# Optimization experiments

Hardware: AMD Instinct MI355X
Metric: run time of the kernel (lower is better)

## Reference

```python
import jax, jax.numpy as jnp
import numpy as np

N = 4096      # n_nodes
IN = 256      # in_features
H = 4         # n_heads
F = 64        # out_features (per head)
SLOPE = 0.2   # leaky relu negative slope


def setup_inputs() -> dict:
    key = jax.random.key(0)
    k0, k1, k2, k3 = jax.random.split(key, 4)
    h = jax.random.normal(k0, (N, IN), dtype=jnp.float32)
    adj = jax.random.randint(k1, (N, N), 0, 2, dtype=jnp.int32)
    # ensure every node has at least one neighbor (self-loop) so softmax is defined
    adj = jnp.maximum(adj, jnp.eye(N, dtype=jnp.int32))
    # linear: in_features -> out_features * n_heads (xavier-ish scale)
    W = jax.random.normal(k2, (H * F, IN), dtype=jnp.float32) * np.float32(1.0 / np.sqrt(IN))
    b = jnp.zeros((H * F,), dtype=jnp.float32)
    # attn: Linear(2*F -> 1), weight row vector of size 2F plus scalar bias
    attn_w = jax.random.normal(k3, (2 * F,), dtype=jnp.float32) * np.float32(1.0 / np.sqrt(2 * F))
    attn_b = jnp.zeros((1,), dtype=jnp.float32)
    return {"h": h, "adj_mat": adj, "W": W, "b": b, "attn_w": attn_w, "attn_b": attn_b}


def reference(h, adj_mat, W, b, attn_w, attn_b):
    n = h.shape[0]
    # node projection: [N, H, F]
    g = (h @ W.T + b).reshape(n, H, F)
    # attn(concat(h_i, h_j)) = <a_src, g_i> + <a_dst, g_j> + bias  (decomposed, same math)
    src = jnp.einsum('nhf,f->nh', g, attn_w[:F])   # [N, H] contribution of node i
    dst = jnp.einsum('nhf,f->nh', g, attn_w[F:])   # [N, H] contribution of node j
    e = src[:, None, :] + dst[None, :, :] + attn_b[0]   # [N, N, H]
    e = jnp.where(e >= 0, e, SLOPE * e)                 # leaky relu
    e = jnp.where(adj_mat[:, :, None] != 0, e, -jnp.inf)  # mask non-edges
    a = jax.nn.softmax(e, axis=1)                       # softmax over neighbors j
    out = jnp.einsum('ijh,jhf->ihf', a, g)              # [N, H, F]
    return out.mean(axis=1)                             # average heads -> [N, F]
```

## Files before the change

### kernel.cpp

```cpp
#include <hip/hip_runtime.h>
#include <stdint.h>

constexpr int NODES = 4096;
constexpr int KIN   = 256;
constexpr int NHEAD = 4;
constexpr int NF    = 64;
constexpr int HFQ   = 256;
#define SLOPE 0.2f
#define L2E 1.44269504088896340736f

typedef __attribute__((ext_vector_type(8))) short short8;
typedef __attribute__((ext_vector_type(4))) float floatx4;

static __device__ __forceinline__ unsigned short f2bf(float f) {
  return __builtin_bit_cast(unsigned short, (__bf16)f);
}

__global__ __launch_bounds__(256) void prep_kernel(
    const float* __restrict__ hin, const float* __restrict__ Win,
    unsigned short* __restrict__ hB, unsigned short* __restrict__ WB) {
  int idx = blockIdx.x * 256 + threadIdx.x;
  const int NH4 = (NODES * KIN) / 4;
  const int NW4 = (HFQ * KIN) / 4;
  if (idx < NH4) {
    float4 v = reinterpret_cast<const float4*>(hin)[idx];
    ushort4 o = { f2bf(v.x), f2bf(v.y), f2bf(v.z), f2bf(v.w) };
    reinterpret_cast<ushort4*>(hB)[idx] = o;
  } else if (idx < NH4 + NW4) {
    int j = idx - NH4;
    float4 v = reinterpret_cast<const float4*>(Win)[j];
    ushort4 o = { f2bf(v.x), f2bf(v.y), f2bf(v.z), f2bf(v.w) };
    reinterpret_cast<ushort4*>(WB)[j] = o;
  }
}

__global__ __launch_bounds__(256) void proj_kernel(
    const unsigned short* __restrict__ hB, const unsigned short* __restrict__ WB,
    const float* __restrict__ bias,
    float* __restrict__ g32, unsigned short* __restrict__ gT) {
  int wave = threadIdx.x >> 6, lane = threadIdx.x & 63;
  int tile = blockIdx.x * 4 + wave;
  int mt = tile >> 4, nt = tile & 15;
  int m0 = mt * 16, n0 = nt * 16;
  int r = lane & 15, kg = lane >> 4;
  floatx4 acc = {0.f, 0.f, 0.f, 0.f};
  const short8* Ap = reinterpret_cast<const short8*>(hB + (m0 + r) * KIN + kg * 8);
  const short8* Bp = reinterpret_cast<const short8*>(WB + (n0 + r) * KIN + kg * 8);
#pragma unroll
  for (int kb = 0; kb < 8; ++kb) {
    short8 a = Ap[kb * 4];
    short8 b = Bp[kb * 4];
    acc = __builtin_amdgcn_mfma_f32_16x16x32_bf16(a, b, acc, 0, 0, 0);
  }
  int col = n0 + r;
  float bv = bias[col];
#pragma unroll
  for (int q = 0; q < 4; ++q) {
    int row = m0 + kg * 4 + q;
    float v = acc[q] + bv;
    g32[row * HFQ + col] = v;
    gT[col * NODES + row] = f2bf(v);
  }
}

__global__ __launch_bounds__(256) void srcdst_kernel(
    const float* __restrict__ g32, const float* __restrict__ attn_w,
    const float* __restrict__ attn_b,
    float* __restrict__ src, float* __restrict__ dst) {
  int wave = threadIdx.x >> 6, lane = threadIdx.x & 63;
  int n = blockIdx.x * 4 + wave;
  float aws = attn_w[lane], awd = attn_w[64 + lane];
  float ab = attn_b[0];
#pragma unroll
  for (int hh = 0; hh < NHEAD; ++hh) {
    float v = g32[n * HFQ + hh * NF + lane];
    float s = v * aws, d = v * awd;
#pragma unroll
    for (int m = 32; m >= 1; m >>= 1) {
      s += __shfl_xor(s, m, 64);
      d += __shfl_xor(d, m, 64);
    }
    if (lane == 0) {
      src[n * NHEAD + hh] = s + ab;
      dst[n * NHEAD + hh] = d;
    }
  }
}

__global__ __launch_bounds__(256) void attn_kernel(
    const int* __restrict__ adj, const unsigned short* __restrict__ gT,
    const float* __restrict__ src, const float* __restrict__ dst,
    float* __restrict__ pnum, float* __restrict__ pden, int JP) {
  extern __shared__ char smem[];
  unsigned short* gTl = reinterpret_cast<unsigned short*>(smem);
  float* dstL = reinterpret_cast<float*>(smem + 256 * 80);
  int tid = threadIdx.x;
  int wave = tid >> 6, lane = tid & 63;
  int row_in = lane & 15, kg = lane >> 4;
  int part = blockIdx.y;
  int jstart = part * JP;
  int arow = blockIdx.x * 64 + wave * 16 + row_in;

  for (int idx = tid; idx < NHEAD * JP; idx += 256) {
    int hh = idx / JP, jl = idx - hh * JP;
    dstL[hh * JP + jl] = dst[(jstart + jl) * NHEAD + hh];
  }

  float srcv[NHEAD];
#pragma unroll
  for (int hh = 0; hh < NHEAD; ++hh) srcv[hh] = src[arow * NHEAD + hh];

  floatx4 acc[NHEAD][4];
#pragma unroll
  for (int hh = 0; hh < NHEAD; ++hh)
#pragma unroll
    for (int ft = 0; ft < 4; ++ft) acc[hh][ft] = floatx4{0.f, 0.f, 0.f, 0.f};
  float den[NHEAD] = {0.f, 0.f, 0.f, 0.f};

  __syncthreads();

  int nsteps = JP / 32;
  for (int stp = 0; stp < nsteps; ++stp) {
    int j0l = stp * 32;
    int jg = jstart + j0l;
#pragma unroll
    for (int it = 0; it < 4; ++it) {
      int q = it * 256 + tid;
      int c = q >> 2, jc = q & 3;
      short8 v = *reinterpret_cast<const short8*>(gT + c * NODES + jg + jc * 8);
      *reinterpret_cast<short8*>(gTl + c * 40 + jc * 8) = v;
    }
    int base_adj = arow * NODES + jg + kg * 8;
    int4 a01 = *reinterpret_cast<const int4*>(adj + base_adj);
    int4 a23 = *reinterpret_cast<const int4*>(adj + base_adj + 4);
    __syncthreads();
#pragma unroll
    for (int hh = 0; hh < NHEAD; ++hh) {
      const float* dl = dstL + hh * JP + j0l + kg * 8;
      float4 d01 = *reinterpret_cast<const float4*>(dl);
      float4 d23 = *reinterpret_cast<const float4*>(dl + 4);
      float dv[8] = {d01.x, d01.y, d01.z, d01.w, d23.x, d23.y, d23.z, d23.w};
      int av[8] = {a01.x, a01.y, a01.z, a01.w, a23.x, a23.y, a23.z, a23.w};
      float dsum = 0.f;
      short8 afr;
#pragma unroll
      for (int rr = 0; rr < 8; ++rr) {
        float t = srcv[hh] + dv[rr];
        float u = fmaxf(t, SLOPE * t);
        float p = exp2f(u * L2E);
        float wv = (av[rr] != 0) ? p : 0.f;
        dsum += wv;
        afr[rr] = (short)f2bf(wv);
      }
      den[hh] += dsum;
#pragma unroll
      for (int ft = 0; ft < 4; ++ft) {
        int c = hh * NF + ft * 16 + row_in;
        short8 bfr = *reinterpret_cast<const short8*>(gTl + c * 40 + kg * 8);
        acc[hh][ft] = __builtin_amdgcn_mfma_f32_16x16x32_bf16(afr, bfr, acc[hh][ft], 0, 0, 0);
      }
    }
    __syncthreads();
  }

#pragma unroll
  for (int hh = 0; hh < NHEAD; ++hh) {
    den[hh] += __shfl_xor(den[hh], 16, 64);
    den[hh] += __shfl_xor(den[hh], 32, 64);
  }
  if (kg == 0) {
#pragma unroll
    for (int hh = 0; hh < NHEAD; ++hh)
      pden[part * (NODES * NHEAD) + arow * NHEAD + hh] = den[hh];
  }
#pragma unroll
  for (int hh = 0; hh < NHEAD; ++hh)
#pragma unroll
    for (int ft = 0; ft < 4; ++ft)
#pragma unroll
      for (int q = 0; q < 4; ++q) {
        int row = blockIdx.x * 64 + wave * 16 + kg * 4 + q;
        int col = hh * NF + ft * 16 + row_in;
        pnum[part * (NODES * HFQ) + row * HFQ + col] = acc[hh][ft][q];
      }
}

__global__ __launch_bounds__(256) void combine_kernel(
    const float* __restrict__ pnum, const float* __restrict__ pden,
    float* __restrict__ out, int NP) {
  int idx = blockIdx.x * 256 + threadIdx.x;
  int i = idx >> 6, f = idx & 63;
  float o = 0.f;
#pragma unroll
  for (int hh = 0; hh < NHEAD; ++hh) {
    float num = 0.f, den = 0.f;
    for (int p = 0; p < NP; ++p) {
      num += pnum[p * (NODES * HFQ) + i * HFQ + hh * NF + f];
      den += pden[p * (NODES * NHEAD) + i * NHEAD + hh];
    }
    o += num / den;
  }
  out[idx] = 0.25f * o;
}

extern "C" void kernel_launch(void* const* d_in, const int* in_sizes, int n_in,
                              void* d_out, int out_size, void* d_ws, size_t ws_size,
                              hipStream_t stream) {
  const float* hin = (const float*)d_in[0];
  const int* adj   = (const int*)d_in[1];
  const float* W   = (const float*)d_in[2];
  const float* b   = (const float*)d_in[3];
  const float* aw  = (const float*)d_in[4];
  const float* ab  = (const float*)d_in[5];
  float* out = (float*)d_out;
  char* ws = (char*)d_ws;

  unsigned short* hB  = (unsigned short*)(ws + 0x000000);
  unsigned short* WB  = (unsigned short*)(ws + 0x200000);
  float* g32          = (float*)(ws + 0x400000);
  unsigned short* gT  = (unsigned short*)(ws + 0x800000);
  float* src          = (float*)(ws + 0xA00000);
  float* dst          = (float*)(ws + 0xA10000);
  float* pden         = (float*)(ws + 0xA30000);
  float* pnum         = (float*)(ws + 0xB00000);
  const size_t base = 0xB00000;

  int NP = 2;
  if (ws_size >= base + 8ull * NODES * HFQ * 4) NP = 8;
  else if (ws_size >= base + 4ull * NODES * HFQ * 4) NP = 4;
  int JP = NODES / NP;

  prep_kernel<<<1088, 256, 0, stream>>>(hin, W, hB, WB);
  proj_kernel<<<1024, 256, 0, stream>>>(hB, WB, b, g32, gT);
  srcdst_kernel<<<1024, 256, 0, stream>>>(g32, aw, ab, src, dst);
  size_t smem = 256 * 80 + (size_t)NHEAD * JP * 4;
  attn_kernel<<<dim3(64, NP), 256, smem, stream>>>(adj, gT, src, dst, pnum, pden, JP);
  combine_kernel<<<1024, 256, 0, stream>>>(pnum, pden, out, NP);
}
```

Measured before the change: 81.63 us.

## Factor exp of leaky-relu into precomputed exponentials and use 32x32 MFMA per head

Uses the identity exp(leaky(s+d)) = exp(s)exp(d) or exp(0.2s)exp(0.2d), picked by comparing exp(d) with exp(-s). Those exponentials are precomputed per node, so the hot loop does a select and a multiply instead of an exp. The attention kernel is restructured so each wave handles one head with 32x32x16 MFMAs. It reads a blocked-transposed bf16 g layout straight from global memory, with no shared memory or barriers, and computes the denominator with an MFMA against a ones vector. Risks include overflow or underflow of exp(s) and exp(d) for large logits, since there is no max subtraction, and redundant reads of adj per head wave.

```diff
diff --git a/kernel.cpp b/kernel.cpp
--- a/kernel.cpp
+++ b/kernel.cpp
@@ -11,6 +11,7 @@
 
 typedef __attribute__((ext_vector_type(8))) short short8;
 typedef __attribute__((ext_vector_type(4))) float floatx4;
+typedef __attribute__((ext_vector_type(16))) float f32x16;
 
 static __device__ __forceinline__ unsigned short f2bf(float f) {
   return __builtin_bit_cast(unsigned short, (__bf16)f);
@@ -37,7 +38,7 @@
 __global__ __launch_bounds__(256) void proj_kernel(
     const unsigned short* __restrict__ hB, const unsigned short* __restrict__ WB,
     const float* __restrict__ bias,
-    float* __restrict__ g32, unsigned short* __restrict__ gT) {
+    float* __restrict__ g32, unsigned short* __restrict__ gT2) {
   int wave = threadIdx.x >> 6, lane = threadIdx.x & 63;
   int tile = blockIdx.x * 4 + wave;
   int mt = tile >> 4, nt = tile & 15;
@@ -59,14 +60,14 @@
     int row = m0 + kg * 4 + q;
     float v = acc[q] + bv;
     g32[row * HFQ + col] = v;
-    gT[col * NODES + row] = f2bf(v);
+    gT2[(row >> 5) * (HFQ * 32) + col * 32 + (row & 31)] = f2bf(v);
   }
 }
 
 __global__ __launch_bounds__(256) void srcdst_kernel(
     const float* __restrict__ g32, const float* __restrict__ attn_w,
     const float* __restrict__ attn_b,
-    float* __restrict__ src, float* __restrict__ dst) {
+    float4* __restrict__ srcP, float* __restrict__ ed1P, float* __restrict__ ed2P) {
   int wave = threadIdx.x >> 6, lane = threadIdx.x & 63;
   int n = blockIdx.x * 4 + wave;
   float aws = attn_w[lane], awd = attn_w[64 + lane];
@@ -81,108 +82,88 @@
       d += __shfl_xor(d, m, 64);
     }
     if (lane == 0) {
-      src[n * NHEAD + hh] = s + ab;
-      dst[n * NHEAD + hh] = d;
-    }
-  }
-}
-
-__global__ __launch_bounds__(256) void attn_kernel(
-    const int* __restrict__ adj, const unsigned short* __restrict__ gT,
-    const float* __restrict__ src, const float* __restrict__ dst,
+      s += ab;
+      float4 sp;
+      sp.x = exp2f(s * L2E);
+      sp.y = exp2f(0.2f * s * L2E);
+      sp.z = exp2f(-s * L2E);
+      sp.w = 0.f;
+      srcP[n * NHEAD + hh] = sp;
+      ed1P[hh * NODES + n] = exp2f(d * L2E);
+      ed2P[hh * NODES + n] = exp2f(0.2f * d * L2E);
+    }
+  }
+}
+
+__global__ __launch_bounds__(256, 4) void attn_kernel(
+    const int* __restrict__ adj, const unsigned short* __restrict__ gT2,
+    const float4* __restrict__ srcP,
+    const float* __restrict__ ed1P, const float* __restrict__ ed2P,
     float* __restrict__ pnum, float* __restrict__ pden, int JP) {
-  extern __shared__ char smem[];
-  unsigned short* gTl = reinterpret_cast<unsigned short*>(smem);
-  float* dstL = reinterpret_cast<float*>(smem + 256 * 80);
   int tid = threadIdx.x;
-  int wave = tid >> 6, lane = tid & 63;
-  int row_in = lane & 15, kg = lane >> 4;
-  int part = blockIdx.y;
-  int jstart = part * JP;
-  int arow = blockIdx.x * 64 + wave * 16 + row_in;
-
-  for (int idx = tid; idx < NHEAD * JP; idx += 256) {
-    int hh = idx / JP, jl = idx - hh * JP;
-    dstL[hh * JP + jl] = dst[(jstart + jl) * NHEAD + hh];
-  }
-
-  float srcv[NHEAD];
-#pragma unroll
-  for (int hh = 0; hh < NHEAD; ++hh) srcv[hh] = src[arow * NHEAD + hh];
-
-  floatx4 acc[NHEAD][4];
-#pragma unroll
-  for (int hh = 0; hh < NHEAD; ++hh)
-#pragma unroll
-    for (int ft = 0; ft < 4; ++ft) acc[hh][ft] = floatx4{0.f, 0.f, 0.f, 0.f};
-  float den[NHEAD] = {0.f, 0.f, 0.f, 0.f};
-
-  __syncthreads();
+  int hh = tid >> 6, lane = tid & 63;
+  int il = lane & 31, hi = lane >> 5;
+  int part = blockIdx.y, jstart = part * JP;
+  int i = blockIdx.x * 32 + il;
+
+  float4 sp = srcP[i * NHEAD + hh];
+  float es1 = sp.x, es2 = sp.y, thr = sp.z;
+
+  f32x16 acc0 = {0.f,0.f,0.f,0.f,0.f,0.f,0.f,0.f,0.f,0.f,0.f,0.f,0.f,0.f,0.f,0.f};
+  f32x16 acc1 = acc0, accd = acc0;
+
+  short8 ones;
+#pragma unroll
+  for (int r = 0; r < 8; ++r) ones[r] = (short)0x3F80;
+
+  const float* e1base = ed1P + hh * NODES;
+  const float* e2base = ed2P + hh * NODES;
+  const int* adjrow = adj + (size_t)i * NODES;
+  const unsigned short* tA0 = gT2 + (hh * 64 + il) * 32 + hi * 8;
+  const unsigned short* tA1 = tA0 + 32 * 32;
 
   int nsteps = JP / 32;
   for (int stp = 0; stp < nsteps; ++stp) {
-    int j0l = stp * 32;
-    int jg = jstart + j0l;
-#pragma unroll
-    for (int it = 0; it < 4; ++it) {
-      int q = it * 256 + tid;
-      int c = q >> 2, jc = q & 3;
-      short8 v = *reinterpret_cast<const short8*>(gT + c * NODES + jg + jc * 8);
-      *reinterpret_cast<short8*>(gTl + c * 40 + jc * 8) = v;
-    }
-    int base_adj = arow * NODES + jg + kg * 8;
-    int4 a01 = *reinterpret_cast<const int4*>(adj + base_adj);
-    int4 a23 = *reinterpret_cast<const int4*>(adj + base_adj + 4);
-    __syncthreads();
-#pragma unroll
-    for (int hh = 0; hh < NHEAD; ++hh) {
-      const float* dl = dstL + hh * JP + j0l + kg * 8;
-      float4 d01 = *reinterpret_cast<const float4*>(dl);
-      float4 d23 = *reinterpret_cast<const float4*>(dl + 4);
-      float dv[8] = {d01.x, d01.y, d01.z, d01.w, d23.x, d23.y, d23.z, d23.w};
-      int av[8] = {a01.x, a01.y, a01.z, a01.w, a23.x, a23.y, a23.z, a23.w};
-      float dsum = 0.f;
-      short8 afr;
-#pragma unroll
-      for (int rr = 0; rr < 8; ++rr) {
-        float t = srcv[hh] + dv[rr];
-        float u = fmaxf(t, SLOPE * t);
-        float p = exp2f(u * L2E);
-        float wv = (av[rr] != 0) ? p : 0.f;
-        dsum += wv;
-        afr[rr] = (short)f2bf(wv);
+    int j0 = jstart + stp * 32;
+    size_t toff = (size_t)(j0 >> 5) * (HFQ * 32);
+#pragma unroll
+    for (int ch = 0; ch < 2; ++ch) {
+      int jc = j0 + ch * 16 + hi * 8;
+      float4 e1a = *reinterpret_cast<const float4*>(e1base + jc);
+      float4 e1b = *reinterpret_cast<const float4*>(e1base + jc + 4);
+      float4 e2a = *reinterpret_cast<const float4*>(e2base + jc);
+      float4 e2b = *reinterpret_cast<const float4*>(e2base + jc + 4);
+      int4 aa = *reinterpret_cast<const int4*>(adjrow + jc);
+      int4 ab4 = *reinterpret_cast<const int4*>(adjrow + jc + 4);
+      float e1v[8] = {e1a.x, e1a.y, e1a.z, e1a.w, e1b.x, e1b.y, e1b.z, e1b.w};
+      float e2v[8] = {e2a.x, e2a.y, e2a.z, e2a.w, e2b.x, e2b.y, e2b.z, e2b.w};
+      int   av [8] = {aa.x, aa.y, aa.z, aa.w, ab4.x, ab4.y, ab4.z, ab4.w};
+      short8 bfr;
+#pragma unroll
+      for (int r = 0; r < 8; ++r) {
+        bool sel = e1v[r] >= thr;
+        float w = (sel ? es1 : es2) * (sel ? e1v[r] : e2v[r]);
+        w = (av[r] != 0) ? w : 0.f;
+        bfr[r] = (short)f2bf(w);
       }
-      den[hh] += dsum;
-#pragma unroll
-      for (int ft = 0; ft < 4; ++ft) {
-        int c = hh * NF + ft * 16 + row_in;
-        short8 bfr = *reinterpret_cast<const short8*>(gTl + c * 40 + kg * 8);
-        acc[hh][ft] = __builtin_amdgcn_mfma_f32_16x16x32_bf16(afr, bfr, acc[hh][ft], 0, 0, 0);
-      }
-    }
-    __syncthreads();
-  }
-
-#pragma unroll
-  for (int hh = 0; hh < NHEAD; ++hh) {
-    den[hh] += __shfl_xor(den[hh], 16, 64);
-    den[hh] += __shfl_xor(den[hh], 32, 64);
-  }
-  if (kg == 0) {
-#pragma unroll
-    for (int hh = 0; hh < NHEAD; ++hh)
-      pden[part * (NODES * NHEAD) + arow * NHEAD + hh] = den[hh];
-  }
-#pragma unroll
-  for (int hh = 0; hh < NHEAD; ++hh)
-#pragma unroll
-    for (int ft = 0; ft < 4; ++ft)
-#pragma unroll
-      for (int q = 0; q < 4; ++q) {
-        int row = blockIdx.x * 64 + wave * 16 + kg * 4 + q;
-        int col = hh * NF + ft * 16 + row_in;
-        pnum[part * (NODES * HFQ) + row * HFQ + col] = acc[hh][ft][q];
-      }
+      const short8 a0 = *reinterpret_cast<const short8*>(tA0 + toff + ch * 16);
+      const short8 a1 = *reinterpret_cast<const short8*>(tA1 + toff + ch * 16);
+      acc0 = __builtin_amdgcn_mfma_f32_32x32x16_bf16(a0, bfr, acc0, 0, 0, 0);
+      acc1 = __builtin_amdgcn_mfma_f32_32x32x16_bf16(a1, bfr, acc1, 0, 0, 0);
+      accd = __builtin_amdgcn_mfma_f32_32x32x16_bf16(ones, bfr, accd, 0, 0, 0);
+    }
+  }
+
+  if (hi == 0)
+    pden[(size_t)part * (NODES * NHEAD) + i * NHEAD + hh] = accd[0];
+
+  float* pbase = pnum + (size_t)part * (NODES * HFQ) + (size_t)i * HFQ + hh * NF;
+#pragma unroll
+  for (int reg = 0; reg < 16; ++reg) {
+    int crow = (reg & 3) + 8 * (reg >> 2) + 4 * hi;
+    pbase[crow] = acc0[reg];
+    pbase[32 + crow] = acc1[reg];
+  }
 }
 
 __global__ __launch_bounds__(256) void combine_kernel(
@@ -218,10 +199,11 @@
   unsigned short* hB  = (unsigned short*)(ws + 0x000000);
   unsigned short* WB  = (unsigned short*)(ws + 0x200000);
   float* g32          = (float*)(ws + 0x400000);
-  unsigned short* gT  = (unsigned short*)(ws + 0x800000);
-  float* src          = (float*)(ws + 0xA00000);
-  float* dst          = (float*)(ws + 0xA10000);
-  float* pden         = (float*)(ws + 0xA30000);
+  unsigned short* gT2 = (unsigned short*)(ws + 0x800000);
+  float4* srcP        = (float4*)(ws + 0xA00000);
+  float* ed1P         = (float*)(ws + 0xA40000);
+  float* ed2P         = (float*)(ws + 0xA50000);
+  float* pden         = (float*)(ws + 0xA60000);
   float* pnum         = (float*)(ws + 0xB00000);
   const size_t base = 0xB00000;
 
@@ -231,9 +213,8 @@
   int JP = NODES / NP;
 
   prep_kernel<<<1088, 256, 0, stream>>>(hin, W, hB, WB);
-  proj_kernel<<<1024, 256, 0, stream>>>(hB, WB, b, g32, gT);
-  srcdst_kernel<<<1024, 256, 0, stream>>>(g32, aw, ab, src, dst);
-  size_t smem = 256 * 80 + (size_t)NHEAD * JP * 4;
-  attn_kernel<<<dim3(64, NP), 256, smem, stream>>>(adj, gT, src, dst, pnum, pden, JP);
+  proj_kernel<<<1024, 256, 0, stream>>>(hB, WB, b, g32, gT2);
+  srcdst_kernel<<<1024, 256, 0, stream>>>(g32, aw, ab, srcP, ed1P, ed2P);
+  attn_kernel<<<dim3(128, NP), 256, 0, stream>>>(adj, gT2, srcP, ed1P, ed2P, pnum, pden, JP);
   combine_kernel<<<1024, 256, 0, stream>>>(pnum, pden, out, NP);
 }
```

After: 102.3 us. 25.3% more time.
